# Performance work log

Measured on AMD Instinct MI355X. Metric: run time of the kernel, lower is better.

The kernel has to match this reference:

```python
import jax, jax.numpy as jnp
import numpy as np

# Mamba2 defaults (mamba_ssm): expand=2, headdim=64, d_conv=4, ngroups=1
D_MODEL, D_STATE, D_INNER, HEADDIM, D_CONV = 512, 64, 1024, 64, 4
NHEADS = D_INNER // HEADDIM  # 16
CONV_DIM = D_INNER + 2 * D_STATE  # 1152
D_IN_PROJ = 2 * D_INNER + 2 * D_STATE + NHEADS  # 2192
BATCH, SEQLEN = 2, 2048
RMS_EPS = 1.1920929e-07  # torch nn.RMSNorm eps=None -> fp32 machine eps
GNORM_EPS = 1e-5  # mamba_ssm RMSNormGated default


def _rms(t, w, eps):
    return t * jax.lax.rsqrt(jnp.mean(t * t, axis=-1, keepdims=True) + eps) * w


def _mamba2(u, in_w, conv_w, conv_b, dt_bias, A_log, Dp, gnorm_w, out_w):
    """Mamba2 block forward (ngroups=1). u: (b, l, d_model) -> (b, l, d_model)."""
    b, l, _ = u.shape
    zxbcdt = jnp.einsum('bld,ed->ble', u, in_w)  # (b, l, 2192)
    z = zxbcdt[..., :D_INNER]
    xBC = zxbcdt[..., D_INNER:D_INNER + CONV_DIM]
    dt = jax.nn.softplus(zxbcdt[..., -NHEADS:] + dt_bias)  # (b, l, h)
    # causal depthwise conv, kernel D_CONV, then SiLU
    xp = jnp.pad(xBC, ((0, 0), (D_CONV - 1, 0), (0, 0)))
    xBC = conv_b + sum(xp[:, i:i + l, :] * conv_w[:, i] for i in range(D_CONV))
    xBC = jax.nn.silu(xBC)
    x = xBC[..., :D_INNER].reshape(b, l, NHEADS, HEADDIM)
    Bm = xBC[..., D_INNER:D_INNER + D_STATE]  # (b, l, n)
    Cm = xBC[..., D_INNER + D_STATE:]         # (b, l, n)
    dA = jnp.exp(dt * (-jnp.exp(A_log)))      # (b, l, h), decay per head

    def step(h, inp):
        dA_t, dt_t, B_t, C_t, x_t = inp  # (b,h) (b,h) (b,n) (b,n) (b,h,p)
        h = h * dA_t[:, :, None, None] + jnp.einsum('bh,bhp,bn->bhpn', dt_t, x_t, B_t)
        y = jnp.einsum('bhpn,bn->bhp', h, C_t)
        return h, y

    h0 = jnp.zeros((b, NHEADS, HEADDIM, D_STATE), u.dtype)
    xs = (jnp.swapaxes(dA, 0, 1), jnp.swapaxes(dt, 0, 1), jnp.swapaxes(Bm, 0, 1),
          jnp.swapaxes(Cm, 0, 1), jnp.swapaxes(x, 0, 1))
    _, ys = jax.lax.scan(step, h0, xs)  # (l, b, h, p)
    y = jnp.swapaxes(ys, 0, 1) + x * Dp[None, None, :, None]
    y = y.reshape(b, l, D_INNER)
    # gated RMSNorm: norm(y * silu(z)) * weight
    y = y * jax.nn.silu(z)
    y = _rms(y, gnorm_w, GNORM_EPS)
    return jnp.einsum('bli,oi->blo', y, out_w)


def _layer(x, pos_emb, pixel_mask, norm_ssm_w, norm_ffn_w, ffn_w1, ffn_b1, ffn_w2, ffn_b2,
           f_in_w, f_conv_w, f_conv_b, f_dt_bias, f_A_log, f_D, f_gnorm_w, f_out_w,
           b_in_w, b_conv_w, b_conv_b, b_dt_bias, b_A_log, b_D, b_gnorm_w, b_out_w):
    si = _rms(x, norm_ssm_w, RMS_EPS) + pos_emb
    fwd = _mamba2(si, f_in_w, f_conv_w, f_conv_b, f_dt_bias, f_A_log, f_D, f_gnorm_w, f_out_w)
    bwd = jnp.flip(_mamba2(jnp.flip(si, 1), b_in_w, b_conv_w, b_conv_b, b_dt_bias,
                           b_A_log, b_D, b_gnorm_w, b_out_w), 1)
    ssm_out = (fwd + bwd) * pixel_mask[..., None]  # merge='add'
    x = x + ssm_out
    h = _rms(x, norm_ffn_w, RMS_EPS)
    h = jax.nn.gelu(h @ ffn_w1.T + ffn_b1, approximate=False)
    return x + (h @ ffn_w2.T + ffn_b2)


def setup_inputs() -> dict:
    key = jax.random.key(0)
    ks = jax.random.split(key, 16)
    f32 = jnp.float32
    inp = {}
    inp['x'] = jax.random.normal(ks[0], (BATCH, SEQLEN, D_MODEL), f32)
    inp['pos_emb'] = jax.random.normal(ks[1], (BATCH, SEQLEN, D_MODEL), f32) * 0.02
    inp['pixel_mask'] = jnp.ones((BATCH, SEQLEN), f32)
    inp['norm_ssm_w'] = jnp.ones((D_MODEL,), f32)
    inp['norm_ffn_w'] = jnp.ones((D_MODEL,), f32)
    d_ffn = 4 * D_MODEL
    inp['ffn_w1'] = jax.random.normal(ks[2], (d_ffn, D_MODEL), f32) * 0.02
    inp['ffn_b1'] = jnp.zeros((d_ffn,), f32)
    inp['ffn_w2'] = jax.random.normal(ks[3], (D_MODEL, d_ffn), f32) * 0.02
    inp['ffn_b2'] = jnp.zeros((D_MODEL,), f32)
    i = 4
    for pre in ('f', 'b'):
        inp[pre + '_in_w'] = jax.random.normal(ks[i], (D_IN_PROJ, D_MODEL), f32) * 0.02; i += 1
        inp[pre + '_conv_w'] = jax.random.uniform(ks[i], (CONV_DIM, D_CONV), f32, -0.5, 0.5); i += 1
        inp[pre + '_conv_b'] = jnp.zeros((CONV_DIM,), f32)
        dt0 = jnp.exp(jax.random.uniform(ks[i], (NHEADS,), f32) * (jnp.log(0.1) - jnp.log(0.001)) + jnp.log(0.001)); i += 1
        inp[pre + '_dt_bias'] = dt0 + jnp.log(-jnp.expm1(-dt0))  # inverse softplus
        inp[pre + '_A_log'] = jnp.log(jax.random.uniform(ks[i], (NHEADS,), f32, 1.0, 16.0)); i += 1
        inp[pre + '_D'] = jnp.ones((NHEADS,), f32)
        inp[pre + '_gnorm_w'] = jnp.ones((D_INNER,), f32)
        inp[pre + '_out_w'] = jax.random.normal(ks[i], (D_MODEL, D_INNER), f32) * 0.02; i += 1
    return inp


def reference(x, pos_emb, pixel_mask, norm_ssm_w, norm_ffn_w, ffn_w1, ffn_b1, ffn_w2, ffn_b2,
              f_in_w, f_conv_w, f_conv_b, f_dt_bias, f_A_log, f_D, f_gnorm_w, f_out_w,
              b_in_w, b_conv_w, b_conv_b, b_dt_bias, b_A_log, b_D, b_gnorm_w, b_out_w):
    return _layer(x, pos_emb, pixel_mask, norm_ssm_w, norm_ffn_w, ffn_w1, ffn_b1, ffn_w2, ffn_b2,
                  f_in_w, f_conv_w, f_conv_b, f_dt_bias, f_A_log, f_D, f_gnorm_w, f_out_w,
                  b_in_w, b_conv_w, b_conv_b, b_dt_bias, b_A_log, b_D, b_gnorm_w, b_out_w)
```

## Files before the change

kernel.cpp:

```cpp
#include <hip/hip_runtime.h>
#include <hip/hip_bf16.h>

typedef unsigned short u16;
typedef unsigned int u32;
typedef __bf16 bf16x8 __attribute__((ext_vector_type(8)));
typedef float f32x4 __attribute__((ext_vector_type(4)));

typedef __attribute__((address_space(1))) void gvoid_t;
typedef __attribute__((address_space(3))) void lvoid_t;
__device__ __forceinline__ void lds_cp16(void* lds, const void* g) {
    __builtin_amdgcn_global_load_lds((gvoid_t*)g, (lvoid_t*)lds, 16, 0, 0);
}

__device__ __forceinline__ float bf2f(u16 v) {
    u32 x = (u32)v << 16;
    return __builtin_bit_cast(float, x);
}
__device__ __forceinline__ u16 f2bf(float f) {
    return __builtin_bit_cast(u16, (__bf16)f);
}

__device__ __forceinline__ float block_sum_256(float v, float* red) {
    #pragma unroll
    for (int o = 32; o > 0; o >>= 1) v += __shfl_xor(v, o);
    int w = threadIdx.x >> 6;
    if ((threadIdx.x & 63) == 0) red[w] = v;
    __syncthreads();
    return red[0] + red[1] + red[2] + red[3];
}

__global__ __launch_bounds__(256) void k_prep(
    const float* __restrict__ f_inw, const float* __restrict__ b_inw,
    const float* __restrict__ f_ow, const float* __restrict__ b_ow,
    const float* __restrict__ w1, const float* __restrict__ w2,
    u16* __restrict__ INWF, u16* __restrict__ INWB,
    u16* __restrict__ OWF, u16* __restrict__ OWB,
    u16* __restrict__ W1B, u16* __restrict__ W2B,
    const float* __restrict__ x, const float* __restrict__ pe,
    const float* __restrict__ wrms, u16* __restrict__ sib) {
    if (blockIdx.x < 21504) {
        int i = blockIdx.x * 256 + threadIdx.x;
        if (i < 1179648) { int n = i >> 9; INWF[i] = (n < 2192) ? f2bf(f_inw[i]) : (u16)0; return; }
        i -= 1179648;
        if (i < 1179648) { int n = i >> 9; INWB[i] = (n < 2192) ? f2bf(b_inw[i]) : (u16)0; return; }
        i -= 1179648;
        if (i < 524288) { OWF[i] = f2bf(f_ow[i]); return; }
        i -= 524288;
        if (i < 524288) { OWB[i] = f2bf(b_ow[i]); return; }
        i -= 524288;
        if (i < 1048576) { W1B[i] = f2bf(w1[i]); return; }
        i -= 1048576;
        if (i < 1048576) W2B[i] = f2bf(w2[i]);
        return;
    }
    __shared__ float red[4];
    int row = blockIdx.x - 21504, t = threadIdx.x;
    size_t base = (size_t)row * 512 + t * 2;
    float2 xv = *(const float2*)(x + base);
    float ss = block_sum_256(xv.x * xv.x + xv.y * xv.y, red);
    float sc = rsqrtf(ss * (1.f / 512.f) + 1.1920929e-07f);
    float2 pv = *(const float2*)(pe + base);
    float2 wv = *(const float2*)(wrms + t * 2);
    sib[base] = f2bf(xv.x * sc * wv.x + pv.x);
    sib[base + 1] = f2bf(xv.y * sc * wv.y + pv.y);
}

__global__ __launch_bounds__(256) void k_gemm_in(
    const u16* __restrict__ A, const u16* __restrict__ W0, const u16* __restrict__ W1,
    u16* __restrict__ Z0, u16* __restrict__ Z1,
    u16* __restrict__ XB0, u16* __restrict__ XB1) {
    const int z = blockIdx.z;
    const u16* W = z ? W1 : W0;
    u16* Z = z ? Z1 : Z0;
    u16* XB = z ? XB1 : XB0;
    const int K = 512;

    __shared__ __align__(16) u16 As[2][128 * 32];
    __shared__ __align__(16) u16 Bs[2][128 * 32];

    const int t = threadIdx.x;
    const int lane = t & 63;
    const int w = t >> 6;
    const int m0 = blockIdx.y * 128;
    const int n0 = blockIdx.x * 128;
    const int wm = (w >> 1) * 64;
    const int wn = (w & 1) * 64;
    const int fr = lane & 15;
    const int fk = (lane >> 4) * 8;

    f32x4 acc[4][4];
    #pragma unroll
    for (int i = 0; i < 4; ++i)
        #pragma unroll
        for (int j = 0; j < 4; ++j) acc[i][j] = (f32x4){0.f, 0.f, 0.f, 0.f};

    auto STAGE = [&](int buf, int kt) {
        #pragma unroll
        for (int j = 0; j < 2; ++j) {
            int off16 = j * 256 + t;
            int row = off16 >> 2;
            int kc = (off16 & 3) * 8;
            int gm = m0 + row;
            if (z) gm = (gm & ~2047) | (2047 - (gm & 2047));
            lds_cp16(As[buf] + off16 * 8, A + (size_t)gm * K + kt + kc);
            lds_cp16(Bs[buf] + off16 * 8, W + (size_t)(n0 + row) * K + kt + kc);
        }
    };

    STAGE(0, 0);
    __syncthreads();
    int cur = 0;
    for (int kt = 0; kt < K; kt += 32) {
        if (kt + 32 < K) STAGE(cur ^ 1, kt + 32);
        bf16x8 af[4], bfr[4];
        #pragma unroll
        for (int i = 0; i < 4; ++i) af[i] = *(const bf16x8*)(As[cur] + (wm + i * 16 + fr) * 32 + fk);
        #pragma unroll
        for (int i = 0; i < 4; ++i) bfr[i] = *(const bf16x8*)(Bs[cur] + (wn + i * 16 + fr) * 32 + fk);
        #pragma unroll
        for (int i = 0; i < 4; ++i)
            #pragma unroll
            for (int j = 0; j < 4; ++j)
                acc[i][j] = __builtin_amdgcn_mfma_f32_16x16x32_bf16(af[i], bfr[j], acc[i][j], 0, 0, 0);
        __syncthreads();
        cur ^= 1;
    }
    #pragma unroll
    for (int i = 0; i < 4; ++i) {
        int rbase = m0 + wm + i * 16 + (lane >> 4) * 4;
        #pragma unroll
        for (int j = 0; j < 4; ++j) {
            int c = n0 + wn + j * 16 + fr;
            #pragma unroll
            for (int r = 0; r < 4; ++r) {
                u16 v = f2bf(acc[i][j][r]);
                int m = rbase + r;
                if (c < 1024) Z[(size_t)m * 1024 + c] = v;
                else if (c < 2192) XB[(size_t)m * 1184 + (c - 1024)] = v;
            }
        }
    }
}

template <int EPI>
__global__ __launch_bounds__(256) void k_gemm128(
    const u16* __restrict__ A0, const u16* __restrict__ A1,
    const u16* __restrict__ W0, const u16* __restrict__ W1,
    u16* __restrict__ C0, u16* __restrict__ C1, int N, int K,
    const float* __restrict__ bias, const float* __restrict__ resid,
    float* __restrict__ outf) {
    const int z = blockIdx.z;
    const u16* A = z ? A1 : A0;
    const u16* W = z ? W1 : W0;
    u16* C = z ? C1 : C0;

    __shared__ __align__(16) u16 As[2][128 * 32];
    __shared__ __align__(16) u16 Bs[2][128 * 32];

    const int t = threadIdx.x;
    const int lane = t & 63;
    const int w = t >> 6;
    const int m0 = blockIdx.y * 128;
    const int n0 = blockIdx.x * 128;
    const int wm = (w >> 1) * 64;
    const int wn = (w & 1) * 64;
    const int fr = lane & 15;
    const int fk = (lane >> 4) * 8;

    f32x4 acc[4][4];
    #pragma unroll
    for (int i = 0; i < 4; ++i)
        #pragma unroll
        for (int j = 0; j < 4; ++j) acc[i][j] = (f32x4){0.f, 0.f, 0.f, 0.f};

    auto STAGE = [&](int buf, int kt) {
        #pragma unroll
        for (int j = 0; j < 2; ++j) {
            int off16 = j * 256 + t;
            int row = off16 >> 2;
            int kc = (off16 & 3) * 8;
            lds_cp16(As[buf] + off16 * 8, A + (size_t)(m0 + row) * K + kt + kc);
            lds_cp16(Bs[buf] + off16 * 8, W + (size_t)(n0 + row) * K + kt + kc);
        }
    };

    STAGE(0, 0);
    __syncthreads();
    int cur = 0;
    for (int kt = 0; kt < K; kt += 32) {
        if (kt + 32 < K) STAGE(cur ^ 1, kt + 32);
        bf16x8 af[4], bfr[4];
        #pragma unroll
        for (int i = 0; i < 4; ++i) af[i] = *(const bf16x8*)(As[cur] + (wm + i * 16 + fr) * 32 + fk);
        #pragma unroll
        for (int i = 0; i < 4; ++i) bfr[i] = *(const bf16x8*)(Bs[cur] + (wn + i * 16 + fr) * 32 + fk);
        #pragma unroll
        for (int i = 0; i < 4; ++i)
            #pragma unroll
            for (int j = 0; j < 4; ++j)
                acc[i][j] = __builtin_amdgcn_mfma_f32_16x16x32_bf16(af[i], bfr[j], acc[i][j], 0, 0, 0);
        __syncthreads();
        cur ^= 1;
    }
    #pragma unroll
    for (int i = 0; i < 4; ++i) {
        int rbase = m0 + wm + i * 16 + (lane >> 4) * 4;
        #pragma unroll
        for (int j = 0; j < 4; ++j) {
            int col = n0 + wn + j * 16 + fr;
            #pragma unroll
            for (int r = 0; r < 4; ++r) {
                int m = rbase + r;
                float v = acc[i][j][r];
                if (EPI == 0) {
                    C[(size_t)m * N + col] = f2bf(v);
                } else if (EPI == 1) {
                    float xg = v + bias[col];
                    C[(size_t)m * N + col] = f2bf(0.5f * xg * (1.f + erff(xg * 0.70710678118654752f)));
                } else {
                    outf[(size_t)m * N + col] = v + bias[col] + resid[(size_t)m * N + col];
                }
            }
        }
    }
}

template <int EPI>
__global__ __launch_bounds__(256) void k_gemm12864(
    const u16* __restrict__ A0, const u16* __restrict__ A1,
    const u16* __restrict__ W0, const u16* __restrict__ W1,
    u16* __restrict__ C0, u16* __restrict__ C1, int N, int K,
    const float* __restrict__ bias, const float* __restrict__ resid,
    float* __restrict__ outf) {
    const int z = blockIdx.z;
    const u16* A = z ? A1 : A0;
    const u16* W = z ? W1 : W0;
    u16* C = z ? C1 : C0;

    __shared__ __align__(16) u16 As[2][128 * 32];
    __shared__ __align__(16) u16 Bs[2][64 * 32];

    const int t = threadIdx.x;
    const int lane = t & 63;
    const int w = t >> 6;
    const int m0 = blockIdx.y * 128;
    const int n0 = blockIdx.x * 64;
    const int wm = w * 32;
    const int fr = lane & 15;
    const int fk = (lane >> 4) * 8;

    f32x4 acc[2][4];
    #pragma unroll
    for (int i = 0; i < 2; ++i)
        #pragma unroll
        for (int j = 0; j < 4; ++j) acc[i][j] = (f32x4){0.f, 0.f, 0.f, 0.f};

    auto STAGE = [&](int buf, int kt) {
        #pragma unroll
        for (int j = 0; j < 2; ++j) {
            int off16 = j * 256 + t;
            int row = off16 >> 2;
            int kc = (off16 & 3) * 8;
            lds_cp16(As[buf] + off16 * 8, A + (size_t)(m0 + row) * K + kt + kc);
        }
        lds_cp16(Bs[buf] + t * 8, W + (size_t)(n0 + (t >> 2)) * K + kt + (t & 3) * 8);
    };

    STAGE(0, 0);
    __syncthreads();
    int cur = 0;
    for (int kt = 0; kt < K; kt += 32) {
        if (kt + 32 < K) STAGE(cur ^ 1, kt + 32);
        bf16x8 af[2], bfr[4];
        #pragma unroll
        for (int i = 0; i < 2; ++i) af[i] = *(const bf16x8*)(As[cur] + (wm + i * 16 + fr) * 32 + fk);
        #pragma unroll
        for (int j = 0; j < 4; ++j) bfr[j] = *(const bf16x8*)(Bs[cur] + (j * 16 + fr) * 32 + fk);
        #pragma unroll
        for (int i = 0; i < 2; ++i)
            #pragma unroll
            for (int j = 0; j < 4; ++j)
                acc[i][j] = __builtin_amdgcn_mfma_f32_16x16x32_bf16(af[i], bfr[j], acc[i][j], 0, 0, 0);
        __syncthreads();
        cur ^= 1;
    }
    #pragma unroll
    for (int i = 0; i < 2; ++i) {
        int rbase = m0 + wm + i * 16 + (lane >> 4) * 4;
        #pragma unroll
        for (int j = 0; j < 4; ++j) {
            int col = n0 + j * 16 + fr;
            #pragma unroll
            for (int r = 0; r < 4; ++r) {
                int m = rbase + r;
                float v = acc[i][j][r];
                if (EPI == 0) {
                    C[(size_t)m * N + col] = f2bf(v);
                } else if (EPI == 1) {
                    float xg = v + bias[col];
                    C[(size_t)m * N + col] = f2bf(0.5f * xg * (1.f + erff(xg * 0.70710678118654752f)));
                } else {
                    outf[(size_t)m * N + col] = v + bias[col] + resid[(size_t)m * N + col];
                }
            }
        }
    }
}

template <int EPI>
__global__ __launch_bounds__(256) void k_gemm64(
    const u16* __restrict__ A0, const u16* __restrict__ A1,
    const u16* __restrict__ W0, const u16* __restrict__ W1,
    u16* __restrict__ C0, u16* __restrict__ C1, int N, int K,
    const float* __restrict__ bias, const float* __restrict__ resid,
    float* __restrict__ outf) {
    const int z = blockIdx.z;
    const u16* A = z ? A1 : A0;
    const u16* W = z ? W1 : W0;
    u16* C = z ? C1 : C0;

    __shared__ __align__(16) u16 As[2][64 * 32];
    __shared__ __align__(16) u16 Bs[2][64 * 32];

    const int t = threadIdx.x;
    const int lane = t & 63;
    const int w = t >> 6;
    const int m0 = blockIdx.y * 64;
    const int n0 = blockIdx.x * 64;
    const int wm = (w >> 1) * 32;
    const int wn = (w & 1) * 32;
    const int fr = lane & 15;
    const int fk = (lane >> 4) * 8;

    f32x4 acc[2][2];
    #pragma unroll
    for (int i = 0; i < 2; ++i)
        #pragma unroll
        for (int j = 0; j < 2; ++j) acc[i][j] = (f32x4){0.f, 0.f, 0.f, 0.f};

    const int srow = t >> 2;
    const int skc = (t & 3) * 8;
    auto STAGE = [&](int buf, int kt) {
        lds_cp16(As[buf] + t * 8, A + (size_t)(m0 + srow) * K + kt + skc);
        lds_cp16(Bs[buf] + t * 8, W + (size_t)(n0 + srow) * K + kt + skc);
    };

    STAGE(0, 0);
    __syncthreads();
    int cur = 0;
    for (int kt = 0; kt < K; kt += 32) {
        if (kt + 32 < K) STAGE(cur ^ 1, kt + 32);
        bf16x8 af[2], bfr[2];
        #pragma unroll
        for (int i = 0; i < 2; ++i) af[i] = *(const bf16x8*)(As[cur] + (wm + i * 16 + fr) * 32 + fk);
        #pragma unroll
        for (int j = 0; j < 2; ++j) bfr[j] = *(const bf16x8*)(Bs[cur] + (wn + j * 16 + fr) * 32 + fk);
        #pragma unroll
        for (int i = 0; i < 2; ++i)
            #pragma unroll
            for (int j = 0; j < 2; ++j)
                acc[i][j] = __builtin_amdgcn_mfma_f32_16x16x32_bf16(af[i], bfr[j], acc[i][j], 0, 0, 0);
        __syncthreads();
        cur ^= 1;
    }
    #pragma unroll
    for (int i = 0; i < 2; ++i) {
        int rbase = m0 + wm + i * 16 + (lane >> 4) * 4;
        #pragma unroll
        for (int j = 0; j < 2; ++j) {
            int col = n0 + wn + j * 16 + fr;
            #pragma unroll
            for (int r = 0; r < 4; ++r) {
                int m = rbase + r;
                float v = acc[i][j][r];
                if (EPI == 0) {
                    C[(size_t)m * N + col] = f2bf(v);
                } else if (EPI == 1) {
                    float xg = v + bias[col];
                    C[(size_t)m * N + col] = f2bf(0.5f * xg * (1.f + erff(xg * 0.70710678118654752f)));
                } else {
                    outf[(size_t)m * N + col] = v + bias[col] + resid[(size_t)m * N + col];
                }
            }
        }
    }
}

__global__ __launch_bounds__(160) void k_conv(
    const u16* __restrict__ xb0, const u16* __restrict__ xb1,
    const float* __restrict__ cw0, const float* __restrict__ cb0,
    const float* __restrict__ dtb0, const float* __restrict__ al0,
    const float* __restrict__ cw1, const float* __restrict__ cb1,
    const float* __restrict__ dtb1, const float* __restrict__ al1,
    u16* __restrict__ xc0, u16* __restrict__ xc1,
    float* __restrict__ dtO0, float* __restrict__ dAO0,
    float* __restrict__ dtO1, float* __restrict__ dAO1) {
    int g = blockIdx.x;
    int dir = g >> 9;
    int row0 = (g & 511) * 8;
    const u16* xb = dir ? xb1 : xb0;
    const float* cw = dir ? cw1 : cw0;
    const float* cb = dir ? cb1 : cb0;
    const float* dtb = dir ? dtb1 : dtb0;
    const float* al = dir ? al1 : al0;
    u16* xc = dir ? xc1 : xc0;
    float* dtO = dir ? dtO1 : dtO0;
    float* dAO = dir ? dAO1 : dAO0;
    int tl0 = row0 & 2047;
    int rbatch = row0 - tl0;
    int t = threadIdx.x;
    if (t < 144) {
        int col = t * 8;
        float cwa[8][4];
        #pragma unroll
        for (int j = 0; j < 8; ++j) {
            float4 c4 = *(const float4*)(cw + (col + j) * 4);
            cwa[j][0] = c4.x; cwa[j][1] = c4.y; cwa[j][2] = c4.z; cwa[j][3] = c4.w;
        }
        float cbv[8];
        float4 cb0v = *(const float4*)(cb + col);
        float4 cb1v = *(const float4*)(cb + col + 4);
        cbv[0] = cb0v.x; cbv[1] = cb0v.y; cbv[2] = cb0v.z; cbv[3] = cb0v.w;
        cbv[4] = cb1v.x; cbv[5] = cb1v.y; cbv[6] = cb1v.z; cbv[7] = cb1v.w;
        uint4 win[4];
        win[0] = win[1] = win[2] = make_uint4(0, 0, 0, 0);
        #pragma unroll
        for (int i = 0; i < 3; ++i) {
            int tt = tl0 - 3 + i;
            if (tt >= 0) win[i] = *(const uint4*)(xb + (size_t)(rbatch + tt) * 1184 + col);
        }
        for (int s = 0; s < 8; ++s) {
            win[3] = *(const uint4*)(xb + (size_t)(rbatch + tl0 + s) * 1184 + col);
            const u16* w0 = (const u16*)&win[0];
            const u16* w1 = (const u16*)&win[1];
            const u16* w2 = (const u16*)&win[2];
            const u16* w3 = (const u16*)&win[3];
            u16 ov[8];
            #pragma unroll
            for (int j = 0; j < 8; ++j) {
                float a = cbv[j] + bf2f(w0[j]) * cwa[j][0] + bf2f(w1[j]) * cwa[j][1]
                        + bf2f(w2[j]) * cwa[j][2] + bf2f(w3[j]) * cwa[j][3];
                ov[j] = f2bf(a / (1.f + expf(-a)));
            }
            *(uint4*)(xc + (size_t)(row0 + s) * 1152 + col) = *(const uint4*)ov;
            win[0] = win[1]; win[1] = win[2]; win[2] = win[3];
        }
    } else if (t < 160) {
        int hh = t - 144;
        float nal = -expf(al[hh]);
        float dtbv = dtb[hh];
        for (int s = 0; s < 8; ++s) {
            int row = row0 + s;
            float v = bf2f(xb[(size_t)row * 1184 + 1152 + hh]) + dtbv;
            float sp = (v > 20.f) ? v : log1pf(expf(v));
            dtO[row * 16 + hh] = sp;
            dAO[row * 16 + hh] = nal * sp;
        }
    }
}

__global__ __launch_bounds__(256) void k_ssd_state(
    const u16* __restrict__ xc0, const float* __restrict__ dt0, const float* __restrict__ ld0,
    const u16* __restrict__ xc1, const float* __restrict__ dt1, const float* __restrict__ ld1,
    float* __restrict__ S, float* __restrict__ Aprod) {
    int blk = blockIdx.x;
    int c = blk & 31, h = (blk >> 5) & 15, b = (blk >> 9) & 1, dir = blk >> 10;
    const u16* xc = dir ? xc1 : xc0;
    const float* dtp = dir ? dt1 : dt0;
    const float* ldp = dir ? ld1 : ld0;
    const int t = threadIdx.x, w = t >> 6, lane = t & 63;
    const int fr = lane & 15, fk = (lane >> 4) * 8;

    __shared__ __align__(16) u16 sBt[64 * 72];
    __shared__ __align__(16) u16 sXp[64 * 72];
    __shared__ float ssc[64];
    size_t row0 = (size_t)b * 2048 + c * 64;

    if (t < 64) {
        float v = ldp[(row0 + t) * 16 + h];
        float dtv = dtp[(row0 + t) * 16 + h];
        #pragma unroll
        for (int o = 1; o < 64; o <<= 1) {
            float u = __shfl_up(v, o);
            if (lane >= o) v += u;
        }
        float last = __shfl(v, 63);
        ssc[t] = dtv * expf(last - v);
        if (t == 63) Aprod[blk] = expf(v);
    }
    __syncthreads();
    #pragma unroll
    for (int i2 = t; i2 < 512; i2 += 256) {
        int r = i2 >> 3, e8 = (i2 & 7) * 8;
        size_t rb = (row0 + r) * 1152;
        uint4 bv = *(const uint4*)(xc + rb + 1024 + e8);
        uint4 xv = *(const uint4*)(xc + rb + h * 64 + e8);
        const u16* bs = (const u16*)&bv;
        const u16* xs = (const u16*)&xv;
        float sc = ssc[r];
        #pragma unroll
        for (int j = 0; j < 8; ++j) {
            sBt[(e8 + j) * 72 + r] = bs[j];
            sXp[(e8 + j) * 72 + r] = f2bf(bf2f(xs[j]) * sc);
        }
    }
    __syncthreads();

    f32x4 acc[4];
    #pragma unroll
    for (int j = 0; j < 4; ++j) acc[j] = (f32x4){0.f, 0.f, 0.f, 0.f};
    #pragma unroll
    for (int k0 = 0; k0 < 64; k0 += 32) {
        bf16x8 a = *(const bf16x8*)(sBt + (w * 16 + fr) * 72 + k0 + fk);
        #pragma unroll
        for (int j = 0; j < 4; ++j) {
            bf16x8 bb = *(const bf16x8*)(sXp + (j * 16 + fr) * 72 + k0 + fk);
            acc[j] = __builtin_amdgcn_mfma_f32_16x16x32_bf16(a, bb, acc[j], 0, 0, 0);
        }
    }
    float* Sb = S + (size_t)blk * 4096;
    int nb = w * 16 + (lane >> 4) * 4;
    #pragma unroll
    for (int j = 0; j < 4; ++j) {
        int p = j * 16 + fr;
        *(f32x4*)(Sb + p * 64 + nb) = acc[j];
    }
}

__global__ __launch_bounds__(256) void k_scan_carry(float* __restrict__ S,
                                                    const float* __restrict__ Aprod) {
    int g = blockIdx.x;
    int blk = g >> 4;
    int e = (g & 15) * 256 + threadIdx.x;
    size_t base = (size_t)blk * 32 * 4096 + e;
    float sv[32];
    #pragma unroll
    for (int c = 0; c < 32; ++c) sv[c] = S[base + (size_t)c * 4096];
    float ap[32];
    #pragma unroll
    for (int c = 0; c < 32; ++c) ap[c] = Aprod[blk * 32 + c];
    float h = 0.f;
    #pragma unroll
    for (int c = 0; c < 32; ++c) {
        S[base + (size_t)c * 4096] = h;
        h = ap[c] * h + sv[c];
    }
}

__global__ __launch_bounds__(256) void k_ssd_y(
    const u16* __restrict__ xc0, const float* __restrict__ dt0, const float* __restrict__ ld0,
    const float* __restrict__ Dv0, u16* __restrict__ y0,
    const u16* __restrict__ xc1, const float* __restrict__ dt1, const float* __restrict__ ld1,
    const float* __restrict__ Dv1, u16* __restrict__ y1,
    const float* __restrict__ S) {
    int blk = blockIdx.x;
    int c = blk & 31, h = (blk >> 5) & 15, b = (blk >> 9) & 1, dir = blk >> 10;
    const u16* xc = dir ? xc1 : xc0;
    const float* dtp = dir ? dt1 : dt0;
    const float* ldp = dir ? ld1 : ld0;
    u16* y = dir ? y1 : y0;
    const float Dh = (dir ? Dv1 : Dv0)[h];
    const int t = threadIdx.x, w = t >> 6, lane = t & 63;
    const int fr = lane & 15, fk = (lane >> 4) * 8;

    __shared__ __align__(16) u16 sB[64 * 72];
    __shared__ __align__(16) u16 sC[64 * 72];
    __shared__ __align__(16) u16 sXp[64 * 72];
    __shared__ __align__(16) u16 sHi[64 * 72];
    __shared__ __align__(16) u16 sLo[64 * 72];
    __shared__ __align__(16) u16 sGl[64 * 72];
    __shared__ float scl[64], sdt[64];
    size_t row0 = (size_t)b * 2048 + c * 64;

    if (t < 64) {
        float v = ldp[(row0 + t) * 16 + h];
        float dtv = dtp[(row0 + t) * 16 + h];
        #pragma unroll
        for (int o = 1; o < 64; o <<= 1) {
            float u = __shfl_up(v, o);
            if (lane >= o) v += u;
        }
        scl[t] = v;
        sdt[t] = dtv;
    }
    __syncthreads();
    #pragma unroll
    for (int i2 = t; i2 < 512; i2 += 256) {
        int r = i2 >> 3, e8 = (i2 & 7) * 8;
        size_t rb = (row0 + r) * 1152;
        *(uint4*)(sB + r * 72 + e8) = *(const uint4*)(xc + rb + 1024 + e8);
        *(uint4*)(sC + r * 72 + e8) = *(const uint4*)(xc + rb + 1088 + e8);
        uint4 xv = *(const uint4*)(xc + rb + h * 64 + e8);
        const u16* xs = (const u16*)&xv;
        float dtv = sdt[r];
        #pragma unroll
        for (int j = 0; j < 8; ++j) sXp[(e8 + j) * 72 + r] = f2bf(bf2f(xs[j]) * dtv);
    }
    #pragma unroll
    for (int i4 = t; i4 < 1024; i4 += 256) {
        int p = i4 >> 4, n4 = (i4 & 15) * 4;
        float4 hv = *(const float4*)(S + (size_t)blk * 4096 + p * 64 + n4);
        ushort4 hi4, lo4;
        hi4.x = f2bf(hv.x); lo4.x = f2bf(hv.x - bf2f(hi4.x));
        hi4.y = f2bf(hv.y); lo4.y = f2bf(hv.y - bf2f(hi4.y));
        hi4.z = f2bf(hv.z); lo4.z = f2bf(hv.z - bf2f(hi4.z));
        hi4.w = f2bf(hv.w); lo4.w = f2bf(hv.w - bf2f(hi4.w));
        *(ushort4*)(sHi + p * 72 + n4) = hi4;
        *(ushort4*)(sLo + p * 72 + n4) = lo4;
    }
    __syncthreads();

    f32x4 g[4], acc2[4];
    #pragma unroll
    for (int j = 0; j < 4; ++j) { g[j] = (f32x4){0.f,0.f,0.f,0.f}; acc2[j] = (f32x4){0.f,0.f,0.f,0.f}; }
    #pragma unroll
    for (int k0 = 0; k0 < 64; k0 += 32) {
        bf16x8 a = *(const bf16x8*)(sC + (w * 16 + fr) * 72 + k0 + fk);
        #pragma unroll
        for (int j = 0; j < 4; ++j) {
            bf16x8 bb = *(const bf16x8*)(sB + (j * 16 + fr) * 72 + k0 + fk);
            g[j] = __builtin_amdgcn_mfma_f32_16x16x32_bf16(a, bb, g[j], 0, 0, 0);
            bf16x8 bh = *(const bf16x8*)(sHi + (j * 16 + fr) * 72 + k0 + fk);
            acc2[j] = __builtin_amdgcn_mfma_f32_16x16x32_bf16(a, bh, acc2[j], 0, 0, 0);
            bf16x8 bl = *(const bf16x8*)(sLo + (j * 16 + fr) * 72 + k0 + fk);
            acc2[j] = __builtin_amdgcn_mfma_f32_16x16x32_bf16(a, bl, acc2[j], 0, 0, 0);
        }
    }
    #pragma unroll
    for (int j = 0; j < 4; ++j) {
        int r = j * 16 + fr;
        #pragma unroll
        for (int reg = 0; reg < 4; ++reg) {
            int s = w * 16 + (lane >> 4) * 4 + reg;
            float val = (r <= s) ? expf(scl[s] - scl[r]) * g[j][reg] : 0.f;
            sGl[s * 72 + r] = f2bf(val);
        }
    }
    __syncthreads();

    f32x4 acc1[4];
    #pragma unroll
    for (int j = 0; j < 4; ++j) acc1[j] = (f32x4){0.f, 0.f, 0.f, 0.f};
    #pragma unroll
    for (int k0 = 0; k0 < 64; k0 += 32) {
        bf16x8 a = *(const bf16x8*)(sGl + (w * 16 + fr) * 72 + k0 + fk);
        #pragma unroll
        for (int j = 0; j < 4; ++j) {
            bf16x8 bb = *(const bf16x8*)(sXp + (j * 16 + fr) * 72 + k0 + fk);
            acc1[j] = __builtin_amdgcn_mfma_f32_16x16x32_bf16(a, bb, acc1[j], 0, 0, 0);
        }
    }
    #pragma unroll
    for (int reg = 0; reg < 4; ++reg) {
        int s = w * 16 + (lane >> 4) * 4 + reg;
        float es = expf(scl[s]);
        size_t yrb = (row0 + s) * 1024 + h * 64;
        size_t xrb = (row0 + s) * 1152 + h * 64;
        #pragma unroll
        for (int j = 0; j < 4; ++j) {
            int p = j * 16 + fr;
            float xv = bf2f(xc[xrb + p]);
            y[yrb + p] = f2bf(acc1[j][reg] + es * acc2[j][reg] + xv * Dh);
        }
    }
}

__global__ __launch_bounds__(256) void k_gnorm(
    const u16* __restrict__ y0, const u16* __restrict__ z0,
    const float* __restrict__ gw0, u16* __restrict__ o0,
    const u16* __restrict__ y1, const u16* __restrict__ z1,
    const float* __restrict__ gw1, u16* __restrict__ o1) {
    __shared__ float red[4];
    int r = blockIdx.x;
    int dir = r >> 12, row = r & 4095;
    int t = threadIdx.x;
    const u16* y = dir ? y1 : y0;
    const u16* zp = dir ? z1 : z0;
    const float* gw = dir ? gw1 : gw0;
    u16* o = dir ? o1 : o0;
    ushort4 yv = *(const ushort4*)(y + (size_t)row * 1024 + t * 4);
    ushort4 zr = *(const ushort4*)(zp + (size_t)row * 1024 + t * 4);
    float z0f = bf2f(zr.x), z1f = bf2f(zr.y), z2f = bf2f(zr.z), z3f = bf2f(zr.w);
    float v0 = bf2f(yv.x) * (z0f / (1.f + expf(-z0f)));
    float v1 = bf2f(yv.y) * (z1f / (1.f + expf(-z1f)));
    float v2 = bf2f(yv.z) * (z2f / (1.f + expf(-z2f)));
    float v3 = bf2f(yv.w) * (z3f / (1.f + expf(-z3f)));
    float ss = block_sum_256(v0 * v0 + v1 * v1 + v2 * v2 + v3 * v3, red);
    float sc = rsqrtf(ss * (1.f / 1024.f) + 1e-5f);
    float4 gv = *(const float4*)(gw + t * 4);
    size_t ob = (size_t)row * 1024 + t * 4;
    o[ob + 0] = f2bf(v0 * sc * gv.x);
    o[ob + 1] = f2bf(v1 * sc * gv.y);
    o[ob + 2] = f2bf(v2 * sc * gv.z);
    o[ob + 3] = f2bf(v3 * sc * gv.w);
}

__global__ __launch_bounds__(256) void k_add_rms(
    const float* __restrict__ x, const u16* __restrict__ of,
    const u16* __restrict__ ob, const float* __restrict__ mask,
    const float* __restrict__ wrms,
    float* __restrict__ x2, u16* __restrict__ o) {
    __shared__ float red[4];
    int row = blockIdx.x, t = threadIdx.x;
    int bb = row >> 11, tl = row & 2047;
    size_t fb = (size_t)((bb << 11) + (2047 - tl)) * 512;
    float m = mask[row];
    size_t base = (size_t)row * 512 + t * 2;
    size_t fo = fb + t * 2;
    float2 xv = *(const float2*)(x + base);
    float v0 = xv.x + (bf2f(of[base]) + bf2f(ob[fo])) * m;
    float v1 = xv.y + (bf2f(of[base + 1]) + bf2f(ob[fo + 1])) * m;
    x2[base] = v0;
    x2[base + 1] = v1;
    float ss = block_sum_256(v0 * v0 + v1 * v1, red);
    float sc = rsqrtf(ss * (1.f / 512.f) + 1.1920929e-07f);
    float2 wv = *(const float2*)(wrms + t * 2);
    o[base] = f2bf(v0 * sc * wv.x);
    o[base + 1] = f2bf(v1 * sc * wv.y);
}

extern "C" void kernel_launch(void* const* d_in, const int* in_sizes, int n_in,
                              void* d_out, int out_size, void* d_ws, size_t ws_size,
                              hipStream_t stream) {
    const float* x = (const float*)d_in[0];
    const float* pe = (const float*)d_in[1];
    const float* mask = (const float*)d_in[2];
    const float* nsw = (const float*)d_in[3];
    const float* nfw = (const float*)d_in[4];
    const float* w1 = (const float*)d_in[5];
    const float* b1 = (const float*)d_in[6];
    const float* w2 = (const float*)d_in[7];
    const float* b2 = (const float*)d_in[8];
    const float* f_inw = (const float*)d_in[9];
    const float* f_cw = (const float*)d_in[10];
    const float* f_cb = (const float*)d_in[11];
    const float* f_dtb = (const float*)d_in[12];
    const float* f_al = (const float*)d_in[13];
    const float* f_D = (const float*)d_in[14];
    const float* f_gw = (const float*)d_in[15];
    const float* f_ow = (const float*)d_in[16];
    const float* b_inw = (const float*)d_in[17];
    const float* b_cw = (const float*)d_in[18];
    const float* b_cb = (const float*)d_in[19];
    const float* b_dtb = (const float*)d_in[20];
    const float* b_al = (const float*)d_in[21];
    const float* b_D = (const float*)d_in[22];
    const float* b_gw = (const float*)d_in[23];
    const float* b_ow = (const float*)d_in[24];
    float* out = (float*)d_out;

    char* ws = (char*)d_ws;
    u16* Z0   = (u16*)(ws + 0);
    u16* Z1   = (u16*)(ws + 8388608);
    u16* XB0  = (u16*)(ws + 16777216);
    u16* XB1  = (u16*)(ws + 26476544);
    u16* INWF = (u16*)(ws + 36175872);
    u16* INWB = (u16*)(ws + 38535168);
    u16* SIB  = (u16*)(ws + 40894464);
    u16* XC0  = (u16*)(ws + 36175872);
    u16* XC1  = (u16*)(ws + 45613056);
    float* dtF = (float*)(ws + 55050240);
    float* dAF = (float*)(ws + 55312384);
    float* dtB = (float*)(ws + 55574528);
    float* dAB = (float*)(ws + 55836672);
    u16* Y0   = (u16*)(ws + 16777216);
    u16* Y1   = (u16*)(ws + 25165824);
    u16* YG0  = (u16*)(ws + 36175872);
    u16* YG1  = (u16*)(ws + 44564480);
    u16* OP0  = (u16*)(ws + 0);
    u16* OP1  = (u16*)(ws + 4194304);
    float* X2 = (float*)(ws + 8388608);
    u16* X2B  = (u16*)(ws + 0);
    u16* HACT = (u16*)(ws + 16777216);
    u16* OWF = (u16*)(ws + 56098816);
    u16* OWB = (u16*)(ws + 57147392);
    u16* W1B = (u16*)(ws + 58195968);
    u16* W2B = (u16*)(ws + 60293120);
    float* SBUF = (float*)(ws + 62390272);
    float* APR  = (float*)(ws + 95944704);

    k_prep<<<25600, 256, 0, stream>>>(f_inw, b_inw, f_ow, b_ow, w1, w2,
                                      INWF, INWB, OWF, OWB, W1B, W2B,
                                      x, pe, nsw, SIB);
    k_gemm_in<<<dim3(18, 32, 2), 256, 0, stream>>>(SIB, INWF, INWB, Z0, Z1, XB0, XB1);
    k_conv<<<1024, 160, 0, stream>>>(XB0, XB1, f_cw, f_cb, f_dtb, f_al,
                                     b_cw, b_cb, b_dtb, b_al,
                                     XC0, XC1, dtF, dAF, dtB, dAB);
    k_ssd_state<<<2048, 256, 0, stream>>>(XC0, dtF, dAF, XC1, dtB, dAB, SBUF, APR);
    k_scan_carry<<<1024, 256, 0, stream>>>(SBUF, APR);
    k_ssd_y<<<2048, 256, 0, stream>>>(XC0, dtF, dAF, f_D, Y0,
                                      XC1, dtB, dAB, b_D, Y1, SBUF);
    k_gnorm<<<8192, 256, 0, stream>>>(Y0, Z0, f_gw, YG0, Y1, Z1, b_gw, YG1);
    k_gemm12864<0><<<dim3(8, 32, 2), 256, 0, stream>>>(YG0, YG1, OWF, OWB, OP0, OP1, 512, 1024,
                                                       nullptr, nullptr, nullptr);
    k_add_rms<<<4096, 256, 0, stream>>>(x, OP0, OP1, mask, nfw, X2, X2B);
    k_gemm128<1><<<dim3(16, 32, 1), 256, 0, stream>>>(X2B, X2B, W1B, W1B, HACT, HACT, 2048, 512,
                                                      b1, nullptr, nullptr);
    k_gemm64<2><<<dim3(8, 64, 1), 256, 0, stream>>>(HACT, HACT, W2B, W2B, nullptr, nullptr,
                                                    512, 2048, b2, X2, out);
}
```

Measured before the change: 335.6 us.

## Swizzle GEMM LDS layout and vectorize row-norm kernels to one wave per row

Applies an XOR swizzle to the k-chunk position in the LDS tiles of all four GEMM kernels, matching it on the global_load_lds staging side and the fragment read side, to cut LDS bank conflicts on the MFMA operand loads. The prep, gated-norm and add-RMS kernels are rewritten so each wave handles one row with 16-byte vector loads and stores and a shuffle-only reduction, removing the shared-memory reduction and __syncthreads. Weight conversion is vectorized to four elements per thread, so fewer blocks are launched. The swizzle must agree exactly between writer and reader, or results are corrupted.

Result: faster. 328.7 us (-2.0%).

```diff
diff --git a/kernel.cpp b/kernel.cpp
--- a/kernel.cpp
+++ b/kernel.cpp
@@ -20,13 +20,17 @@
     return __builtin_bit_cast(u16, (__bf16)f);
 }
 
-__device__ __forceinline__ float block_sum_256(float v, float* red) {
+__device__ __forceinline__ float wave_sum(float v) {
     #pragma unroll
     for (int o = 32; o > 0; o >>= 1) v += __shfl_xor(v, o);
-    int w = threadIdx.x >> 6;
-    if ((threadIdx.x & 63) == 0) red[w] = v;
-    __syncthreads();
-    return red[0] + red[1] + red[2] + red[3];
+    return v;
+}
+
+__device__ __forceinline__ void cvt4(const float* __restrict__ s, u16* __restrict__ d) {
+    float4 v = *(const float4*)s;
+    ushort4 o;
+    o.x = f2bf(v.x); o.y = f2bf(v.y); o.z = f2bf(v.z); o.w = f2bf(v.w);
+    *(ushort4*)d = o;
 }
 
 __global__ __launch_bounds__(256) void k_prep(
@@ -38,31 +42,55 @@
     u16* __restrict__ W1B, u16* __restrict__ W2B,
     const float* __restrict__ x, const float* __restrict__ pe,
     const float* __restrict__ wrms, u16* __restrict__ sib) {
-    if (blockIdx.x < 21504) {
-        int i = blockIdx.x * 256 + threadIdx.x;
-        if (i < 1179648) { int n = i >> 9; INWF[i] = (n < 2192) ? f2bf(f_inw[i]) : (u16)0; return; }
-        i -= 1179648;
-        if (i < 1179648) { int n = i >> 9; INWB[i] = (n < 2192) ? f2bf(b_inw[i]) : (u16)0; return; }
-        i -= 1179648;
-        if (i < 524288) { OWF[i] = f2bf(f_ow[i]); return; }
-        i -= 524288;
-        if (i < 524288) { OWB[i] = f2bf(b_ow[i]); return; }
-        i -= 524288;
-        if (i < 1048576) { W1B[i] = f2bf(w1[i]); return; }
-        i -= 1048576;
-        if (i < 1048576) W2B[i] = f2bf(w2[i]);
+    if (blockIdx.x < 5376) {
+        int g = blockIdx.x * 256 + threadIdx.x;
+        if (g < 294912) {
+            int i = g * 4, n = i >> 9;
+            if (n < 2192) cvt4(f_inw + i, INWF + i);
+            else *(ushort4*)(INWF + i) = make_ushort4(0, 0, 0, 0);
+            return;
+        }
+        g -= 294912;
+        if (g < 294912) {
+            int i = g * 4, n = i >> 9;
+            if (n < 2192) cvt4(b_inw + i, INWB + i);
+            else *(ushort4*)(INWB + i) = make_ushort4(0, 0, 0, 0);
+            return;
+        }
+        g -= 294912;
+        if (g < 131072) { cvt4(f_ow + g * 4, OWF + g * 4); return; }
+        g -= 131072;
+        if (g < 131072) { cvt4(b_ow + g * 4, OWB + g * 4); return; }
+        g -= 131072;
+        if (g < 262144) { cvt4(w1 + g * 4, W1B + g * 4); return; }
+        g -= 262144;
+        cvt4(w2 + g * 4, W2B + g * 4);
         return;
     }
-    __shared__ float red[4];
-    int row = blockIdx.x - 21504, t = threadIdx.x;
-    size_t base = (size_t)row * 512 + t * 2;
-    float2 xv = *(const float2*)(x + base);
-    float ss = block_sum_256(xv.x * xv.x + xv.y * xv.y, red);
+    int row = (blockIdx.x - 5376) * 4 + (threadIdx.x >> 6);
+    int lane = threadIdx.x & 63;
+    size_t base = (size_t)row * 512 + lane * 4;
+    float4 xa = *(const float4*)(x + base);
+    float4 xb = *(const float4*)(x + base + 256);
+    float ss = xa.x * xa.x + xa.y * xa.y + xa.z * xa.z + xa.w * xa.w
+             + xb.x * xb.x + xb.y * xb.y + xb.z * xb.z + xb.w * xb.w;
+    ss = wave_sum(ss);
     float sc = rsqrtf(ss * (1.f / 512.f) + 1.1920929e-07f);
-    float2 pv = *(const float2*)(pe + base);
-    float2 wv = *(const float2*)(wrms + t * 2);
-    sib[base] = f2bf(xv.x * sc * wv.x + pv.x);
-    sib[base + 1] = f2bf(xv.y * sc * wv.y + pv.y);
+    float4 pa = *(const float4*)(pe + base);
+    float4 pb = *(const float4*)(pe + base + 256);
+    float4 wa = *(const float4*)(wrms + lane * 4);
+    float4 wb = *(const float4*)(wrms + lane * 4 + 256);
+    ushort4 oa, obv;
+    oa.x = f2bf(xa.x * sc * wa.x + pa.x);
+    oa.y = f2bf(xa.y * sc * wa.y + pa.y);
+    oa.z = f2bf(xa.z * sc * wa.z + pa.z);
+    oa.w = f2bf(xa.w * sc * wa.w + pa.w);
+    obv.x = f2bf(xb.x * sc * wb.x + pb.x);
+    obv.y = f2bf(xb.y * sc * wb.y + pb.y);
+    obv.z = f2bf(xb.z * sc * wb.z + pb.z);
+    obv.w = f2bf(xb.w * sc * wb.w + pb.w);
+    *(ushort4*)(sib + base) = oa;
+    *(ushort4*)(sib + base + 256) = obv;
 }
 
 __global__ __launch_bounds__(256) void k_gemm_in(
@@ -86,7 +114,7 @@
     const int wm = (w >> 1) * 64;
     const int wn = (w & 1) * 64;
     const int fr = lane & 15;
-    const int fk = (lane >> 4) * 8;
+    const int ksw = (((lane >> 4) ^ ((fr >> 1) & 3)) & 3) * 8;
 
     f32x4 acc[4][4];
     #pragma unroll
@@ -99,7 +127,7 @@
         for (int j = 0; j < 2; ++j) {
             int off16 = j * 256 + t;
             int row = off16 >> 2;
-            int kc = (off16 & 3) * 8;
+            int kc = (((off16 & 3) ^ ((row >> 1) & 3)) & 3) * 8;
             int gm = m0 + row;
             if (z) gm = (gm & ~2047) | (2047 - (gm & 2047));
             lds_cp16(As[buf] + off16 * 8, A + (size_t)gm * K + kt + kc);
@@ -114,9 +142,9 @@
         if (kt + 32 < K) STAGE(cur ^ 1, kt + 32);
         bf16x8 af[4], bfr[4];
         #pragma unroll
-        for (int i = 0; i < 4; ++i) af[i] = *(const bf16x8*)(As[cur] + (wm + i * 16 + fr) * 32 + fk);
-        #pragma unroll
-        for (int i = 0; i < 4; ++i) bfr[i] = *(const bf16x8*)(Bs[cur] + (wn + i * 16 + fr) * 32 + fk);
+        for (int i = 0; i < 4; ++i) af[i] = *(const bf16x8*)(As[cur] + (wm + i * 16 + fr) * 32 + ksw);
+        #pragma unroll
+        for (int i = 0; i < 4; ++i) bfr[i] = *(const bf16x8*)(Bs[cur] + (wn + i * 16 + fr) * 32 + ksw);
         #pragma unroll
         for (int i = 0; i < 4; ++i)
             #pragma unroll
@@ -165,7 +193,7 @@
     const int wm = (w >> 1) * 64;
     const int wn = (w & 1) * 64;
     const int fr = lane & 15;
-    const int fk = (lane >> 4) * 8;
+    const int ksw = (((lane >> 4) ^ ((fr >> 1) & 3)) & 3) * 8;
 
     f32x4 acc[4][4];
     #pragma unroll
@@ -178,7 +206,7 @@
         for (int j = 0; j < 2; ++j) {
             int off16 = j * 256 + t;
             int row = off16 >> 2;
-            int kc = (off16 & 3) * 8;
+            int kc = (((off16 & 3) ^ ((row >> 1) & 3)) & 3) * 8;
             lds_cp16(As[buf] + off16 * 8, A + (size_t)(m0 + row) * K + kt + kc);
             lds_cp16(Bs[buf] + off16 * 8, W + (size_t)(n0 + row) * K + kt + kc);
         }
@@ -191,9 +219,9 @@
         if (kt + 32 < K) STAGE(cur ^ 1, kt + 32);
         bf16x8 af[4], bfr[4];
         #pragma unroll
-        for (int i = 0; i < 4; ++i) af[i] = *(const bf16x8*)(As[cur] + (wm + i * 16 + fr) * 32 + fk);
-        #pragma unroll
-        for (int i = 0; i < 4; ++i) bfr[i] = *(const bf16x8*)(Bs[cur] + (wn + i * 16 + fr) * 32 + fk);
+        for (int i = 0; i < 4; ++i) af[i] = *(const bf16x8*)(As[cur] + (wm + i * 16 + fr) * 32 + ksw);
+        #pragma unroll
+        for (int i = 0; i < 4; ++i) bfr[i] = *(const bf16x8*)(Bs[cur] + (wn + i * 16 + fr) * 32 + ksw);
         #pragma unroll
         for (int i = 0; i < 4; ++i)
             #pragma unroll
@@ -247,7 +275,7 @@
     const int n0 = blockIdx.x * 64;
     const int wm = w * 32;
     const int fr = lane & 15;
-    const int fk = (lane >> 4) * 8;
+    const int ksw = (((lane >> 4) ^ ((fr >> 1) & 3)) & 3) * 8;
 
     f32x4 acc[2][4];
     #pragma unroll
@@ -260,10 +288,12 @@
         for (int j = 0; j < 2; ++j) {
             int off16 = j * 256 + t;
             int row = off16 >> 2;
-            int kc = (off16 & 3) * 8;
+            int kc = (((off16 & 3) ^ ((row >> 1) & 3)) & 3) * 8;
             lds_cp16(As[buf] + off16 * 8, A + (size_t)(m0 + row) * K + kt + kc);
         }
-        lds_cp16(Bs[buf] + t * 8, W + (size_t)(n0 + (t >> 2)) * K + kt + (t & 3) * 8);
+        int brow = t >> 2;
+        int bkc = (((t & 3) ^ ((brow >> 1) & 3)) & 3) * 8;
+        lds_cp16(Bs[buf] + t * 8, W + (size_t)(n0 + brow) * K + kt + bkc);
     };
 
     STAGE(0, 0);
@@ -273,9 +303,9 @@
         if (kt + 32 < K) STAGE(cur ^ 1, kt + 32);
         bf16x8 af[2], bfr[4];
         #pragma unroll
-        for (int i = 0; i < 2; ++i) af[i] = *(const bf16x8*)(As[cur] + (wm + i * 16 + fr) * 32 + fk);
-        #pragma unroll
-        for (int j = 0; j < 4; ++j) bfr[j] = *(const bf16x8*)(Bs[cur] + (j * 16 + fr) * 32 + fk);
+        for (int i = 0; i < 2; ++i) af[i] = *(const bf16x8*)(As[cur] + (wm + i * 16 + fr) * 32 + ksw);
+        #pragma unroll
+        for (int j = 0; j < 4; ++j) bfr[j] = *(const bf16x8*)(Bs[cur] + (j * 16 + fr) * 32 + ksw);
         #pragma unroll
         for (int i = 0; i < 2; ++i)
             #pragma unroll
@@ -330,7 +360,7 @@
     const int wm = (w >> 1) * 32;
     const int wn = (w & 1) * 32;
     const int fr = lane & 15;
-    const int fk = (lane >> 4) * 8;
+    const int ksw = (((lane >> 4) ^ ((fr >> 1) & 3)) & 3) * 8;
 
     f32x4 acc[2][2];
     #pragma unroll
@@ -339,7 +369,7 @@
         for (int j = 0; j < 2; ++j) acc[i][j] = (f32x4){0.f, 0.f, 0.f, 0.f};
 
     const int srow = t >> 2;
-    const int skc = (t & 3) * 8;
+    const int skc = (((t & 3) ^ ((srow >> 1) & 3)) & 3) * 8;
     auto STAGE = [&](int buf, int kt) {
         lds_cp16(As[buf] + t * 8, A + (size_t)(m0 + srow) * K + kt + skc);
         lds_cp16(Bs[buf] + t * 8, W + (size_t)(n0 + srow) * K + kt + skc);
@@ -352,9 +382,9 @@
         if (kt + 32 < K) STAGE(cur ^ 1, kt + 32);
         bf16x8 af[2], bfr[2];
         #pragma unroll
-        for (int i = 0; i < 2; ++i) af[i] = *(const bf16x8*)(As[cur] + (wm + i * 16 + fr) * 32 + fk);
-        #pragma unroll
-        for (int j = 0; j < 2; ++j) bfr[j] = *(const bf16x8*)(Bs[cur] + (wn + j * 16 + fr) * 32 + fk);
+        for (int i = 0; i < 2; ++i) af[i] = *(const bf16x8*)(As[cur] + (wm + i * 16 + fr) * 32 + ksw);
+        #pragma unroll
+        for (int j = 0; j < 2; ++j) bfr[j] = *(const bf16x8*)(Bs[cur] + (wn + j * 16 + fr) * 32 + ksw);
         #pragma unroll
         for (int i = 0; i < 2; ++i)
             #pragma unroll
@@ -670,29 +700,56 @@
     const float* __restrict__ gw0, u16* __restrict__ o0,
     const u16* __restrict__ y1, const u16* __restrict__ z1,
     const float* __restrict__ gw1, u16* __restrict__ o1) {
-    __shared__ float red[4];
-    int r = blockIdx.x;
-    int dir = r >> 12, row = r & 4095;
-    int t = threadIdx.x;
+    int idx = blockIdx.x * 4 + (threadIdx.x >> 6);
+    int dir = idx >> 12, row = idx & 4095;
+    int lane = threadIdx.x & 63;
     const u16* y = dir ? y1 : y0;
     const u16* zp = dir ? z1 : z0;
     const float* gw = dir ? gw1 : gw0;
     u16* o = dir ? o1 : o0;
-    ushort4 yv = *(const ushort4*)(y + (size_t)row * 1024 + t * 4);
-    ushort4 zr = *(const ushort4*)(zp + (size_t)row * 1024 + t * 4);
-    float z0f = bf2f(zr.x), z1f = bf2f(zr.y), z2f = bf2f(zr.z), z3f = bf2f(zr.w);
-    float v0 = bf2f(yv.x) * (z0f / (1.f + expf(-z0f)));
-    float v1 = bf2f(yv.y) * (z1f / (1.f + expf(-z1f)));
-    float v2 = bf2f(yv.z) * (z2f / (1.f + expf(-z2f)));
-    float v3 = bf2f(yv.w) * (z3f / (1.f + expf(-z3f)));
-    float ss = block_sum_256(v0 * v0 + v1 * v1 + v2 * v2 + v3 * v3, red);
+    size_t base = (size_t)row * 1024 + lane * 8;
+    uint4 ya = *(const uint4*)(y + base);
+    uint4 yb = *(const uint4*)(y + base + 512);
+    uint4 za = *(const uint4*)(zp + base);
+    uint4 zb = *(const uint4*)(zp + base + 512);
+    const u16* yap = (const u16*)&ya;
+    const u16* ybp = (const u16*)&yb;
+    const u16* zap = (const u16*)&za;
+    const u16* zbp = (const u16*)&zb;
+    float v[16];
+    float ss = 0.f;
+    #pragma unroll
+    for (int j = 0; j < 8; ++j) {
+        float zf = bf2f(zap[j]);
+        v[j] = bf2f(yap[j]) * (zf / (1.f + expf(-zf)));
+        ss += v[j] * v[j];
+    }
+    #pragma unroll
+    for (int j = 0; j < 8; ++j) {
+        float zf = bf2f(zbp[j]);
+        v[8 + j] = bf2f(ybp[j]) * (zf / (1.f + expf(-zf)));
+        ss += v[8 + j] * v[8 + j];
+    }
+    ss = wave_sum(ss);
     float sc = rsqrtf(ss * (1.f / 1024.f) + 1e-5f);
-    float4 gv = *(const float4*)(gw + t * 4);
-    size_t ob = (size_t)row * 1024 + t * 4;
-    o[ob + 0] = f2bf(v0 * sc * gv.x);
-    o[ob + 1] = f2bf(v1 * sc * gv.y);
-    o[ob + 2] = f2bf(v2 * sc * gv.z);
-    o[ob + 3] = f2bf(v3 * sc * gv.w);
+    float4 g0 = *(const float4*)(gw + lane * 8);
+    float4 g1 = *(const float4*)(gw + lane * 8 + 4);
+    float4 g2 = *(const float4*)(gw + 512 + lane * 8);
+    float4 g3 = *(const float4*)(gw + 512 + lane * 8 + 4);
+    const float* gp0 = (const float*)&g0;
+    const float* gp1 = (const float*)&g1;
+    const float* gp2 = (const float*)&g2;
+    const float* gp3 = (const float*)&g3;
+    u16 oa[8], obv[8];
+    #pragma unroll
+    for (int j = 0; j < 4; ++j) {
+        oa[j] = f2bf(v[j] * sc * gp0[j]);
+        oa[4 + j] = f2bf(v[4 + j] * sc * gp1[j]);
+        obv[j] = f2bf(v[8 + j] * sc * gp2[j]);
+        obv[4 + j] = f2bf(v[12 + j] * sc * gp3[j]);
+    }
+    *(uint4*)(o + base) = *(const uint4*)oa;
+    *(uint4*)(o + base + 512) = *(const uint4*)obv;
 }
 
 __global__ __launch_bounds__(256) void k_add_rms(
@@ -700,23 +757,47 @@
     const u16* __restrict__ ob, const float* __restrict__ mask,
     const float* __restrict__ wrms,
     float* __restrict__ x2, u16* __restrict__ o) {
-    __shared__ float red[4];
-    int row = blockIdx.x, t = threadIdx.x;
+    int row = blockIdx.x * 4 + (threadIdx.x >> 6);
+    int lane = threadIdx.x & 63;
     int bb = row >> 11, tl = row & 2047;
     size_t fb = (size_t)((bb << 11) + (2047 - tl)) * 512;
     float m = mask[row];
-    size_t base = (size_t)row * 512 + t * 2;
-    size_t fo = fb + t * 2;
-    float2 xv = *(const float2*)(x + base);
-    float v0 = xv.x + (bf2f(of[base]) + bf2f(ob[fo])) * m;
-    float v1 = xv.y + (bf2f(of[base + 1]) + bf2f(ob[fo + 1])) * m;
-    x2[base] = v0;
-    x2[base + 1] = v1;
-    float ss = block_sum_256(v0 * v0 + v1 * v1, red);
+    size_t base = (size_t)row * 512 + lane * 4;
+    size_t fo = fb + lane * 4;
+    float4 xa = *(const float4*)(x + base);
+    float4 xb = *(const float4*)(x + base + 256);
+    ushort4 fa = *(const ushort4*)(of + base);
+    ushort4 fbv = *(const ushort4*)(of + base + 256);
+    ushort4 ba = *(const ushort4*)(ob + fo);
+    ushort4 bbv = *(const ushort4*)(ob + fo + 256);
+    float va[4], vb[4];
+    va[0] = xa.x + (bf2f(fa.x) + bf2f(ba.x)) * m;
+    va[1] = xa.y + (bf2f(fa.y) + bf2f(ba.y)) * m;
+    va[2] = xa.z + (bf2f(fa.z) + bf2f(ba.z)) * m;
+    va[3] = xa.w + (bf2f(fa.w) + bf2f(ba.w)) * m;
+    vb[0] = xb.x + (bf2f(fbv.x) + bf2f(bbv.x)) * m;
+    vb[1] = xb.y + (bf2f(fbv.y) + bf2f(bbv.y)) * m;
+    vb[2] = xb.z + (bf2f(fbv.z) + bf2f(bbv.z)) * m;
+    vb[3] = xb.w + (bf2f(fbv.w) + bf2f(bbv.w)) * m;
+    *(float4*)(x2 + base) = (float4){va[0], va[1], va[2], va[3]};
+    *(float4*)(x2 + base + 256) = (float4){vb[0], vb[1], vb[2], vb[3]};
+    float ss = va[0]*va[0] + va[1]*va[1] + va[2]*va[2] + va[3]*va[3]
+             + vb[0]*vb[0] + vb[1]*vb[1] + vb[2]*vb[2] + vb[3]*vb[3];
+    ss = wave_sum(ss);
     float sc = rsqrtf(ss * (1.f / 512.f) + 1.1920929e-07f);
-    float2 wv = *(const float2*)(wrms + t * 2);
-    o[base] = f2bf(v0 * sc * wv.x);
-    o[base + 1] = f2bf(v1 * sc * wv.y);
+    float4 wa = *(const float4*)(wrms + lane * 4);
+    float4 wb = *(const float4*)(wrms + lane * 4 + 256);
+    ushort4 oa, obv;
+    oa.x = f2bf(va[0] * sc * wa.x);
+    oa.y = f2bf(va[1] * sc * wa.y);
+    oa.z = f2bf(va[2] * sc * wa.z);
+    oa.w = f2bf(va[3] * sc * wa.w);
+    obv.x = f2bf(vb[0] * sc * wb.x);
+    obv.y = f2bf(vb[1] * sc * wb.y);
+    obv.z = f2bf(vb[2] * sc * wb.z);
+    obv.w = f2bf(vb[3] * sc * wb.w);
+    *(ushort4*)(o + base) = oa;
+    *(ushort4*)(o + base + 256) = obv;
 }
 
 extern "C" void kernel_launch(void* const* d_in, const int* in_sizes, int n_in,
@@ -779,9 +860,9 @@
     float* SBUF = (float*)(ws + 62390272);
     float* APR  = (float*)(ws + 95944704);
 
-    k_prep<<<25600, 256, 0, stream>>>(f_inw, b_inw, f_ow, b_ow, w1, w2,
-                                      INWF, INWB, OWF, OWB, W1B, W2B,
-                                      x, pe, nsw, SIB);
+    k_prep<<<6400, 256, 0, stream>>>(f_inw, b_inw, f_ow, b_ow, w1, w2,
+                                     INWF, INWB, OWF, OWB, W1B, W2B,
+                                     x, pe, nsw, SIB);
     k_gemm_in<<<dim3(18, 32, 2), 256, 0, stream>>>(SIB, INWF, INWB, Z0, Z1, XB0, XB1);
     k_conv<<<1024, 160, 0, stream>>>(XB0, XB1, f_cw, f_cb, f_dtb, f_al,
                                      b_cw, b_cb, b_dtb, b_al,
@@ -790,10 +871,10 @@
     k_scan_carry<<<1024, 256, 0, stream>>>(SBUF, APR);
     k_ssd_y<<<2048, 256, 0, stream>>>(XC0, dtF, dAF, f_D, Y0,
                                       XC1, dtB, dAB, b_D, Y1, SBUF);
-    k_gnorm<<<8192, 256, 0, stream>>>(Y0, Z0, f_gw, YG0, Y1, Z1, b_gw, YG1);
+    k_gnorm<<<2048, 256, 0, stream>>>(Y0, Z0, f_gw, YG0, Y1, Z1, b_gw, YG1);
     k_gemm12864<0><<<dim3(8, 32, 2), 256, 0, stream>>>(YG0, YG1, OWF, OWB, OP0, OP1, 512, 1024,
                                                        nullptr, nullptr, nullptr);
-    k_add_rms<<<4096, 256, 0, stream>>>(x, OP0, OP1, mask, nfw, X2, X2B);
+    k_add_rms<<<1024, 256, 0, stream>>>(x, OP0, OP1, mask, nfw, X2, X2B);
     k_gemm128<1><<<dim3(16, 32, 1), 256, 0, stream>>>(X2B, X2B, W1B, W1B, HACT, HACT, 2048, 512,
                                                       b1, nullptr, nullptr);
     k_gemm64<2><<<dim3(8, 64, 1), 256, 0, stream>>>(HACT, HACT, W2B, W2B, nullptr, nullptr,
```
